# Kernel optimization log

Hardware: AMD Instinct MI355X
Metric: run time of the kernel (lower is better)

Reference implementation:

```python
import jax, jax.numpy as jnp
import numpy as np

CUTOFF = 5.2   # ANI-style radial cutoff (Angstrom); module takes this as a python float
BOX = 100.0    # box edge length for ~100k atoms at liquid-like density


def setup_inputs() -> dict:
    key = jax.random.key(0)
    k1, k2, k3, k4, k5 = jax.random.split(key, 5)
    N = 100_000      # atoms (molecules=1)
    P = 6_400_000    # candidate neighbor pairs (~64 per atom)
    coordinates = jax.random.uniform(k1, (1, N, 3), jnp.float32) * BOX
    species = jax.random.randint(k2, (1, N), 0, 8)
    species = jnp.where(jax.random.uniform(k3, (1, N)) < 0.02, -1, species)
    neighbor_idxs = jax.random.randint(k4, (2, P), 0, N)
    # small PBC shift vectors
    shift_values = jax.random.normal(k5, (P, 3), jnp.float32) * 0.1
    return {"species": species, "coordinates": coordinates,
            "neighbor_idxs": neighbor_idxs, "shift_values": shift_values}


def reference(species, coordinates, neighbor_idxs, shift_values):
    """Fused gather -> diff -> norm -> (dummy-mask & cutoff) screen.

    Faithful to Neighborlist._screen_with_cutoff, except dynamic stream
    compaction (nonzero/index_select) is replaced by fixed-size masking
    (jit-compatible): screened-out pairs get indices=-1, distances=0,
    diff_vectors=0.
    """
    coords = coordinates.reshape(-1, 3)              # [N, 3]
    dummy = species.reshape(-1) == -1                # [N]
    i0, i1 = neighbor_idxs[0], neighbor_idxs[1]      # [P], [P]
    valid = ~(dummy[i0] | dummy[i1])                 # non-dummy pairs

    diff = coords[i0] - coords[i1] + shift_values    # [P, 3]
    dist_sq = jnp.sum(diff * diff, axis=-1)          # [P]
    nonzero = dist_sq > 0
    dist = jnp.where(nonzero, jnp.sqrt(jnp.where(nonzero, dist_sq, 1.0)), 0.0)

    keep = valid & (dist <= CUTOFF)                  # [P] screening mask
    indices = jnp.where(keep, neighbor_idxs, -1)     # [2, P]
    distances = jnp.where(keep, dist, 0.0)           # [P]
    diff_vectors = jnp.where(keep[:, None], diff, 0.0)  # [P, 3]
    return indices, distances, diff_vectors
```

## Files before the change

kernel.cpp:

```cpp
#include <hip/hip_runtime.h>
#include <math.h>

#define CUTOFF_F 5.2f
#define BLOCK 256
#define PPT 8
#define BP (BLOCK * PPT)

typedef float f32x4 __attribute__((ext_vector_type(4)));
typedef int   i32x4 __attribute__((ext_vector_type(4)));

__global__ __launch_bounds__(BLOCK) void pack_atoms_kernel(
    const int*   __restrict__ species,
    const float* __restrict__ coords,
    f32x4*       __restrict__ atoms,
    int N)
{
    const int n = blockIdx.x * blockDim.x + threadIdx.x;
    if (n >= N) return;
    f32x4 a;
    a.x = coords[3l*n]; a.y = coords[3l*n+1]; a.z = coords[3l*n+2];
    a.w = (species[n] == -1) ? -1.0f : 0.0f;
    atoms[n] = a;
}

__global__ __launch_bounds__(BLOCK) void nbr_screen8_lds_kernel(
    const f32x4* __restrict__ atoms,
    const int*   __restrict__ nbr,
    const float* __restrict__ shift,
    float*       __restrict__ out,
    int P)
{
    __shared__ f32x4 lds[6 * BLOCK];
    const int  tid = threadIdx.x;
    const long PB  = (long)blockIdx.x * BP;

    if (PB + BP <= P) {
        const long baseA = PB + (long)tid * 4;
        const long baseB = baseA + (long)BLOCK * 4;

        const i32x4 i0A = __builtin_nontemporal_load(
            reinterpret_cast<const i32x4*>(nbr + baseA));
        const i32x4 i1A = __builtin_nontemporal_load(
            reinterpret_cast<const i32x4*>(nbr + (long)P + baseA));
        const i32x4 i0B = __builtin_nontemporal_load(
            reinterpret_cast<const i32x4*>(nbr + baseB));
        const i32x4 i1B = __builtin_nontemporal_load(
            reinterpret_cast<const i32x4*>(nbr + (long)P + baseB));

        const f32x4* src = reinterpret_cast<const f32x4*>(shift + PB * 3);
        f32x4 sreg[6];
        #pragma unroll
        for (int q = 0; q < 6; ++q)
            sreg[q] = __builtin_nontemporal_load(src + q * BLOCK + tid);

        const int ia[8] = {i0A.x, i0A.y, i0A.z, i0A.w, i0B.x, i0B.y, i0B.z, i0B.w};
        const int ib[8] = {i1A.x, i1A.y, i1A.z, i1A.w, i1B.x, i1B.y, i1B.z, i1B.w};
        f32x4 A[8], B[8];
        #pragma unroll
        for (int k = 0; k < 8; ++k) { A[k] = atoms[ia[k]]; B[k] = atoms[ib[k]]; }

        #pragma unroll
        for (int q = 0; q < 6; ++q)
            lds[q * BLOCK + tid] = sreg[q];
        __syncthreads();

        const f32x4 sA0 = lds[tid*3+0], sA1 = lds[tid*3+1], sA2 = lds[tid*3+2];
        const f32x4 sB0 = lds[3*BLOCK + tid*3+0], sB1 = lds[3*BLOCK + tid*3+1],
                    sB2 = lds[3*BLOCK + tid*3+2];
        const float shf[24] = {sA0.x, sA0.y, sA0.z, sA0.w,
                               sA1.x, sA1.y, sA1.z, sA1.w,
                               sA2.x, sA2.y, sA2.z, sA2.w,
                               sB0.x, sB0.y, sB0.z, sB0.w,
                               sB1.x, sB1.y, sB1.z, sB1.w,
                               sB2.x, sB2.y, sB2.z, sB2.w};

        float oi0[8], oi1[8], od[8], dv[24];
        #pragma unroll
        for (int k = 0; k < 8; ++k) {
            const bool valid = (A[k].w == 0.0f) & (B[k].w == 0.0f);
            const float dx = (A[k].x - B[k].x) + shf[3*k];
            const float dy = (A[k].y - B[k].y) + shf[3*k+1];
            const float dz = (A[k].z - B[k].z) + shf[3*k+2];
            const float d2 = __fadd_rn(__fadd_rn(__fmul_rn(dx, dx),
                                                 __fmul_rn(dy, dy)),
                                       __fmul_rn(dz, dz));
            const float dist = (d2 > 0.0f) ? sqrtf(d2) : 0.0f;
            const bool keep = valid && (dist <= CUTOFF_F);
            oi0[k] = keep ? (float)ia[k] : -1.0f;
            oi1[k] = keep ? (float)ib[k] : -1.0f;
            od[k]  = keep ? dist : 0.0f;
            dv[3*k]   = keep ? dx : 0.0f;
            dv[3*k+1] = keep ? dy : 0.0f;
            dv[3*k+2] = keep ? dz : 0.0f;
        }

        f32x4 w;
        w.x = dv[0];  w.y = dv[1];  w.z = dv[2];  w.w = dv[3];  lds[tid*3+0] = w;
        w.x = dv[4];  w.y = dv[5];  w.z = dv[6];  w.w = dv[7];  lds[tid*3+1] = w;
        w.x = dv[8];  w.y = dv[9];  w.z = dv[10]; w.w = dv[11]; lds[tid*3+2] = w;
        w.x = dv[12]; w.y = dv[13]; w.z = dv[14]; w.w = dv[15]; lds[3*BLOCK + tid*3+0] = w;
        w.x = dv[16]; w.y = dv[17]; w.z = dv[18]; w.w = dv[19]; lds[3*BLOCK + tid*3+1] = w;
        w.x = dv[20]; w.y = dv[21]; w.z = dv[22]; w.w = dv[23]; lds[3*BLOCK + tid*3+2] = w;

        f32x4 v;
        f32x4* o0 = reinterpret_cast<f32x4*>(out);
        f32x4* o1 = reinterpret_cast<f32x4*>(out + (long)P);
        f32x4* o2 = reinterpret_cast<f32x4*>(out + 2l*P);
        v.x = oi0[0]; v.y = oi0[1]; v.z = oi0[2]; v.w = oi0[3];
        __builtin_nontemporal_store(v, o0 + (baseA >> 2));
        v.x = oi0[4]; v.y = oi0[5]; v.z = oi0[6]; v.w = oi0[7];
        __builtin_nontemporal_store(v, o0 + (baseB >> 2));
        v.x = oi1[0]; v.y = oi1[1]; v.z = oi1[2]; v.w = oi1[3];
        __builtin_nontemporal_store(v, o1 + (baseA >> 2));
        v.x = oi1[4]; v.y = oi1[5]; v.z = oi1[6]; v.w = oi1[7];
        __builtin_nontemporal_store(v, o1 + (baseB >> 2));
        v.x = od[0];  v.y = od[1];  v.z = od[2];  v.w = od[3];
        __builtin_nontemporal_store(v, o2 + (baseA >> 2));
        v.x = od[4];  v.y = od[5];  v.z = od[6];  v.w = od[7];
        __builtin_nontemporal_store(v, o2 + (baseB >> 2));

        __syncthreads();

        f32x4* dst = reinterpret_cast<f32x4*>(out + 3l*P + PB*3);
        #pragma unroll
        for (int q = 0; q < 6; ++q)
            __builtin_nontemporal_store(lds[q * BLOCK + tid],
                                        dst + q * BLOCK + tid);
    } else {
        for (long p = PB + tid; p < P; p += BLOCK) {
            const int a = nbr[p], b = nbr[(long)P + p];
            const f32x4 ca = atoms[a], cb = atoms[b];
            const bool valid = (ca.w == 0.0f) & (cb.w == 0.0f);
            const float dx = (ca.x - cb.x) + shift[p*3];
            const float dy = (ca.y - cb.y) + shift[p*3+1];
            const float dz = (ca.z - cb.z) + shift[p*3+2];
            const float d2 = __fadd_rn(__fadd_rn(__fmul_rn(dx, dx),
                                                 __fmul_rn(dy, dy)),
                                       __fmul_rn(dz, dz));
            const float dist = (d2 > 0.0f) ? sqrtf(d2) : 0.0f;
            const bool keep = valid && (dist <= CUTOFF_F);
            out[p]         = keep ? (float)a : -1.0f;
            out[(long)P+p] = keep ? (float)b : -1.0f;
            out[2l*P+p]    = keep ? dist : 0.0f;
            out[3l*P+p*3]   = keep ? dx : 0.0f;
            out[3l*P+p*3+1] = keep ? dy : 0.0f;
            out[3l*P+p*3+2] = keep ? dz : 0.0f;
        }
    }
}

extern "C" void kernel_launch(void* const* d_in, const int* in_sizes, int n_in,
                              void* d_out, int out_size, void* d_ws, size_t ws_size,
                              hipStream_t stream) {
    const int*   species = (const int*)  d_in[0];
    const float* coords  = (const float*)d_in[1];
    const int*   nbr     = (const int*)  d_in[2];
    const float* shift   = (const float*)d_in[3];
    float* out = (float*)d_out;

    const int N = in_sizes[0];
    const int P = in_sizes[2] / 2;

    f32x4* atoms = (f32x4*)d_ws;
    hipLaunchKernelGGL(pack_atoms_kernel, dim3((N + BLOCK - 1) / BLOCK),
                       dim3(BLOCK), 0, stream, species, coords, atoms, N);
    const int grid = (P + BP - 1) / BP;
    hipLaunchKernelGGL(nbr_screen8_lds_kernel, dim3(grid), dim3(BLOCK), 0,
                       stream, atoms, nbr, shift, out, P);
}
```

Before: 93.27 us.

## Convert screen kernel to persistent grid-stride loop with index prefetch

The screening kernel becomes persistent: a fixed grid of up to 1024 blocks walks tiles with a grid-stride loop. Inside the loop it prefetches the neighbor indices for the block's next tile while the current tile's gathers and stores are in flight. The goal is to hide the dependent-load latency of index-then-atom gathers, and to cut block launch and tail effects. In exchange, fewer waves are resident per tile and register pressure rises from the prefetched indices, which may lower occupancy and latency hiding.

```diff
diff --git a/kernel.cpp b/kernel.cpp
--- a/kernel.cpp
+++ b/kernel.cpp
@@ -23,7 +23,7 @@
     atoms[n] = a;
 }
 
-__global__ __launch_bounds__(BLOCK) void nbr_screen8_lds_kernel(
+__global__ __launch_bounds__(BLOCK) void nbr_screen_pipe_kernel(
     const f32x4* __restrict__ atoms,
     const int*   __restrict__ nbr,
     const float* __restrict__ shift,
@@ -31,120 +31,145 @@
     int P)
 {
     __shared__ f32x4 lds[6 * BLOCK];
-    const int  tid = threadIdx.x;
-    const long PB  = (long)blockIdx.x * BP;
+    const int tid    = threadIdx.x;
+    const int nTiles = (P + BP - 1) / BP;
+    const int t0     = blockIdx.x;
+    if (t0 >= nTiles) return;
 
-    if (PB + BP <= P) {
-        const long baseA = PB + (long)tid * 4;
-        const long baseB = baseA + (long)BLOCK * 4;
+    i32x4 c0A, c1A, c0B, c1B;
+    {
+        const long PB = (long)t0 * BP;
+        if (PB + BP <= P) {
+            const long baseA = PB + (long)tid * 4;
+            const long baseB = baseA + (long)BLOCK * 4;
+            c0A = __builtin_nontemporal_load(reinterpret_cast<const i32x4*>(nbr + baseA));
+            c1A = __builtin_nontemporal_load(reinterpret_cast<const i32x4*>(nbr + (long)P + baseA));
+            c0B = __builtin_nontemporal_load(reinterpret_cast<const i32x4*>(nbr + baseB));
+            c1B = __builtin_nontemporal_load(reinterpret_cast<const i32x4*>(nbr + (long)P + baseB));
+        }
+    }
 
-        const i32x4 i0A = __builtin_nontemporal_load(
-            reinterpret_cast<const i32x4*>(nbr + baseA));
-        const i32x4 i1A = __builtin_nontemporal_load(
-            reinterpret_cast<const i32x4*>(nbr + (long)P + baseA));
-        const i32x4 i0B = __builtin_nontemporal_load(
-            reinterpret_cast<const i32x4*>(nbr + baseB));
-        const i32x4 i1B = __builtin_nontemporal_load(
-            reinterpret_cast<const i32x4*>(nbr + (long)P + baseB));
+    for (int t = t0; t < nTiles; t += gridDim.x) {
+        const long PB = (long)t * BP;
+        if (PB + BP <= P) {
+            const long baseA = PB + (long)tid * 4;
+            const long baseB = baseA + (long)BLOCK * 4;
 
-        const f32x4* src = reinterpret_cast<const f32x4*>(shift + PB * 3);
-        f32x4 sreg[6];
-        #pragma unroll
-        for (int q = 0; q < 6; ++q)
-            sreg[q] = __builtin_nontemporal_load(src + q * BLOCK + tid);
+            const int ia[8] = {c0A.x, c0A.y, c0A.z, c0A.w, c0B.x, c0B.y, c0B.z, c0B.w};
+            const int ib[8] = {c1A.x, c1A.y, c1A.z, c1A.w, c1B.x, c1B.y, c1B.z, c1B.w};
 
-        const int ia[8] = {i0A.x, i0A.y, i0A.z, i0A.w, i0B.x, i0B.y, i0B.z, i0B.w};
-        const int ib[8] = {i1A.x, i1A.y, i1A.z, i1A.w, i1B.x, i1B.y, i1B.z, i1B.w};
-        f32x4 A[8], B[8];
-        #pragma unroll
-        for (int k = 0; k < 8; ++k) { A[k] = atoms[ia[k]]; B[k] = atoms[ib[k]]; }
+            f32x4 A[8], B[8];
+            #pragma unroll
+            for (int k = 0; k < 8; ++k) { A[k] = atoms[ia[k]]; B[k] = atoms[ib[k]]; }
 
-        #pragma unroll
-        for (int q = 0; q < 6; ++q)
-            lds[q * BLOCK + tid] = sreg[q];
-        __syncthreads();
+            const f32x4* src = reinterpret_cast<const f32x4*>(shift + PB * 3);
+            f32x4 sreg[6];
+            #pragma unroll
+            for (int q = 0; q < 6; ++q)
+                sreg[q] = __builtin_nontemporal_load(src + q * BLOCK + tid);
 
-        const f32x4 sA0 = lds[tid*3+0], sA1 = lds[tid*3+1], sA2 = lds[tid*3+2];
-        const f32x4 sB0 = lds[3*BLOCK + tid*3+0], sB1 = lds[3*BLOCK + tid*3+1],
-                    sB2 = lds[3*BLOCK + tid*3+2];
-        const float shf[24] = {sA0.x, sA0.y, sA0.z, sA0.w,
-                               sA1.x, sA1.y, sA1.z, sA1.w,
-                               sA2.x, sA2.y, sA2.z, sA2.w,
-                               sB0.x, sB0.y, sB0.z, sB0.w,
-                               sB1.x, sB1.y, sB1.z, sB1.w,
-                               sB2.x, sB2.y, sB2.z, sB2.w};
+            const int  tn   = t + gridDim.x;
+            const long PBn  = (long)tn * BP;
+            i32x4 n0A, n1A, n0B, n1B;
+            const bool pre = (PBn + BP <= P);
+            if (pre) {
+                const long bA = PBn + (long)tid * 4;
+                const long bB = bA + (long)BLOCK * 4;
+                n0A = __builtin_nontemporal_load(reinterpret_cast<const i32x4*>(nbr + bA));
+                n1A = __builtin_nontemporal_load(reinterpret_cast<const i32x4*>(nbr + (long)P + bA));
+                n0B = __builtin_nontemporal_load(reinterpret_cast<const i32x4*>(nbr + bB));
+                n1B = __builtin_nontemporal_load(reinterpret_cast<const i32x4*>(nbr + (long)P + bB));
+            }
 
-        float oi0[8], oi1[8], od[8], dv[24];
-        #pragma unroll
-        for (int k = 0; k < 8; ++k) {
-            const bool valid = (A[k].w == 0.0f) & (B[k].w == 0.0f);
-            const float dx = (A[k].x - B[k].x) + shf[3*k];
-            const float dy = (A[k].y - B[k].y) + shf[3*k+1];
-            const float dz = (A[k].z - B[k].z) + shf[3*k+2];
-            const float d2 = __fadd_rn(__fadd_rn(__fmul_rn(dx, dx),
-                                                 __fmul_rn(dy, dy)),
-                                       __fmul_rn(dz, dz));
-            const float dist = (d2 > 0.0f) ? sqrtf(d2) : 0.0f;
-            const bool keep = valid && (dist <= CUTOFF_F);
-            oi0[k] = keep ? (float)ia[k] : -1.0f;
-            oi1[k] = keep ? (float)ib[k] : -1.0f;
-            od[k]  = keep ? dist : 0.0f;
-            dv[3*k]   = keep ? dx : 0.0f;
-            dv[3*k+1] = keep ? dy : 0.0f;
-            dv[3*k+2] = keep ? dz : 0.0f;
-        }
+            #pragma unroll
+            for (int q = 0; q < 6; ++q)
+                lds[q * BLOCK + tid] = sreg[q];
+            __syncthreads();
 
-        f32x4 w;
-        w.x = dv[0];  w.y = dv[1];  w.z = dv[2];  w.w = dv[3];  lds[tid*3+0] = w;
-        w.x = dv[4];  w.y = dv[5];  w.z = dv[6];  w.w = dv[7];  lds[tid*3+1] = w;
-        w.x = dv[8];  w.y = dv[9];  w.z = dv[10]; w.w = dv[11]; lds[tid*3+2] = w;
-        w.x = dv[12]; w.y = dv[13]; w.z = dv[14]; w.w = dv[15]; lds[3*BLOCK + tid*3+0] = w;
-        w.x = dv[16]; w.y = dv[17]; w.z = dv[18]; w.w = dv[19]; lds[3*BLOCK + tid*3+1] = w;
-        w.x = dv[20]; w.y = dv[21]; w.z = dv[22]; w.w = dv[23]; lds[3*BLOCK + tid*3+2] = w;
+            const f32x4 sA0 = lds[tid*3+0], sA1 = lds[tid*3+1], sA2 = lds[tid*3+2];
+            const f32x4 sB0 = lds[3*BLOCK + tid*3+0], sB1 = lds[3*BLOCK + tid*3+1],
+                        sB2 = lds[3*BLOCK + tid*3+2];
+            const float shf[24] = {sA0.x, sA0.y, sA0.z, sA0.w,
+                                   sA1.x, sA1.y, sA1.z, sA1.w,
+                                   sA2.x, sA2.y, sA2.z, sA2.w,
+                                   sB0.x, sB0.y, sB0.z, sB0.w,
+                                   sB1.x, sB1.y, sB1.z, sB1.w,
+                                   sB2.x, sB2.y, sB2.z, sB2.w};
 
-        f32x4 v;
-        f32x4* o0 = reinterpret_cast<f32x4*>(out);
-        f32x4* o1 = reinterpret_cast<f32x4*>(out + (long)P);
-        f32x4* o2 = reinterpret_cast<f32x4*>(out + 2l*P);
-        v.x = oi0[0]; v.y = oi0[1]; v.z = oi0[2]; v.w = oi0[3];
-        __builtin_nontemporal_store(v, o0 + (baseA >> 2));
-        v.x = oi0[4]; v.y = oi0[5]; v.z = oi0[6]; v.w = oi0[7];
-        __builtin_nontemporal_store(v, o0 + (baseB >> 2));
-        v.x = oi1[0]; v.y = oi1[1]; v.z = oi1[2]; v.w = oi1[3];
-        __builtin_nontemporal_store(v, o1 + (baseA >> 2));
-        v.x = oi1[4]; v.y = oi1[5]; v.z = oi1[6]; v.w = oi1[7];
-        __builtin_nontemporal_store(v, o1 + (baseB >> 2));
-        v.x = od[0];  v.y = od[1];  v.z = od[2];  v.w = od[3];
-        __builtin_nontemporal_store(v, o2 + (baseA >> 2));
-        v.x = od[4];  v.y = od[5];  v.z = od[6];  v.w = od[7];
-        __builtin_nontemporal_store(v, o2 + (baseB >> 2));
+            float oi0[8], oi1[8], od[8], dv[24];
+            #pragma unroll
+            for (int k = 0; k < 8; ++k) {
+                const bool valid = (A[k].w == 0.0f) & (B[k].w == 0.0f);
+                const float dx = (A[k].x - B[k].x) + shf[3*k];
+                const float dy = (A[k].y - B[k].y) + shf[3*k+1];
+                const float dz = (A[k].z - B[k].z) + shf[3*k+2];
+                const float d2 = __fadd_rn(__fadd_rn(__fmul_rn(dx, dx),
+                                                     __fmul_rn(dy, dy)),
+                                           __fmul_rn(dz, dz));
+                const float dist = (d2 > 0.0f) ? sqrtf(d2) : 0.0f;
+                const bool keep = valid && (dist <= CUTOFF_F);
+                oi0[k] = keep ? (float)ia[k] : -1.0f;
+                oi1[k] = keep ? (float)ib[k] : -1.0f;
+                od[k]  = keep ? dist : 0.0f;
+                dv[3*k]   = keep ? dx : 0.0f;
+                dv[3*k+1] = keep ? dy : 0.0f;
+                dv[3*k+2] = keep ? dz : 0.0f;
+            }
 
-        __syncthreads();
+            f32x4 w;
+            w.x = dv[0];  w.y = dv[1];  w.z = dv[2];  w.w = dv[3];  lds[tid*3+0] = w;
+            w.x = dv[4];  w.y = dv[5];  w.z = dv[6];  w.w = dv[7];  lds[tid*3+1] = w;
+            w.x = dv[8];  w.y = dv[9];  w.z = dv[10]; w.w = dv[11]; lds[tid*3+2] = w;
+            w.x = dv[12]; w.y = dv[13]; w.z = dv[14]; w.w = dv[15]; lds[3*BLOCK + tid*3+0] = w;
+            w.x = dv[16]; w.y = dv[17]; w.z = dv[18]; w.w = dv[19]; lds[3*BLOCK + tid*3+1] = w;
+            w.x = dv[20]; w.y = dv[21]; w.z = dv[22]; w.w = dv[23]; lds[3*BLOCK + tid*3+2] = w;
 
-        f32x4* dst = reinterpret_cast<f32x4*>(out + 3l*P + PB*3);
-        #pragma unroll
-        for (int q = 0; q < 6; ++q)
-            __builtin_nontemporal_store(lds[q * BLOCK + tid],
-                                        dst + q * BLOCK + tid);
-    } else {
-        for (long p = PB + tid; p < P; p += BLOCK) {
-            const int a = nbr[p], b = nbr[(long)P + p];
-            const f32x4 ca = atoms[a], cb = atoms[b];
-            const bool valid = (ca.w == 0.0f) & (cb.w == 0.0f);
-            const float dx = (ca.x - cb.x) + shift[p*3];
-            const float dy = (ca.y - cb.y) + shift[p*3+1];
-            const float dz = (ca.z - cb.z) + shift[p*3+2];
-            const float d2 = __fadd_rn(__fadd_rn(__fmul_rn(dx, dx),
-                                                 __fmul_rn(dy, dy)),
-                                       __fmul_rn(dz, dz));
-            const float dist = (d2 > 0.0f) ? sqrtf(d2) : 0.0f;
-            const bool keep = valid && (dist <= CUTOFF_F);
-            out[p]         = keep ? (float)a : -1.0f;
-            out[(long)P+p] = keep ? (float)b : -1.0f;
-            out[2l*P+p]    = keep ? dist : 0.0f;
-            out[3l*P+p*3]   = keep ? dx : 0.0f;
-            out[3l*P+p*3+1] = keep ? dy : 0.0f;
-            out[3l*P+p*3+2] = keep ? dz : 0.0f;
+            f32x4 v;
+            f32x4* o0 = reinterpret_cast<f32x4*>(out);
+            f32x4* o1 = reinterpret_cast<f32x4*>(out + (long)P);
+            f32x4* o2 = reinterpret_cast<f32x4*>(out + 2l*P);
+            v.x = oi0[0]; v.y = oi0[1]; v.z = oi0[2]; v.w = oi0[3];
+            __builtin_nontemporal_store(v, o0 + (baseA >> 2));
+            v.x = oi0[4]; v.y = oi0[5]; v.z = oi0[6]; v.w = oi0[7];
+            __builtin_nontemporal_store(v, o0 + (baseB >> 2));
+            v.x = oi1[0]; v.y = oi1[1]; v.z = oi1[2]; v.w = oi1[3];
+            __builtin_nontemporal_store(v, o1 + (baseA >> 2));
+            v.x = oi1[4]; v.y = oi1[5]; v.z = oi1[6]; v.w = oi1[7];
+            __builtin_nontemporal_store(v, o1 + (baseB >> 2));
+            v.x = od[0];  v.y = od[1];  v.z = od[2];  v.w = od[3];
+            __builtin_nontemporal_store(v, o2 + (baseA >> 2));
+            v.x = od[4];  v.y = od[5];  v.z = od[6];  v.w = od[7];
+            __builtin_nontemporal_store(v, o2 + (baseB >> 2));
+
+            __syncthreads();
+
+            f32x4* dst = reinterpret_cast<f32x4*>(out + 3l*P + PB*3);
+            #pragma unroll
+            for (int q = 0; q < 6; ++q)
+                __builtin_nontemporal_store(lds[q * BLOCK + tid],
+                                            dst + q * BLOCK + tid);
+
+            if (pre) { c0A = n0A; c1A = n1A; c0B = n0B; c1B = n1B; }
+        } else {
+            for (long p = PB + tid; p < P; p += BLOCK) {
+                const int a = nbr[p], b = nbr[(long)P + p];
+                const f32x4 ca = atoms[a], cb = atoms[b];
+                const bool valid = (ca.w == 0.0f) & (cb.w == 0.0f);
+                const float dx = (ca.x - cb.x) + shift[p*3];
+                const float dy = (ca.y - cb.y) + shift[p*3+1];
+                const float dz = (ca.z - cb.z) + shift[p*3+2];
+                const float d2 = __fadd_rn(__fadd_rn(__fmul_rn(dx, dx),
+                                                     __fmul_rn(dy, dy)),
+                                           __fmul_rn(dz, dz));
+                const float dist = (d2 > 0.0f) ? sqrtf(d2) : 0.0f;
+                const bool keep = valid && (dist <= CUTOFF_F);
+                out[p]         = keep ? (float)a : -1.0f;
+                out[(long)P+p] = keep ? (float)b : -1.0f;
+                out[2l*P+p]    = keep ? dist : 0.0f;
+                out[3l*P+p*3]   = keep ? dx : 0.0f;
+                out[3l*P+p*3+1] = keep ? dy : 0.0f;
+                out[3l*P+p*3+2] = keep ? dz : 0.0f;
+            }
         }
     }
 }
@@ -164,7 +189,10 @@
     f32x4* atoms = (f32x4*)d_ws;
     hipLaunchKernelGGL(pack_atoms_kernel, dim3((N + BLOCK - 1) / BLOCK),
                        dim3(BLOCK), 0, stream, species, coords, atoms, N);
-    const int grid = (P + BP - 1) / BP;
-    hipLaunchKernelGGL(nbr_screen8_lds_kernel, dim3(grid), dim3(BLOCK), 0,
+
+    const int nTiles = (P + BP - 1) / BP;
+    int grid = 1024;
+    if (grid > nTiles) grid = nTiles;
+    hipLaunchKernelGGL(nbr_screen_pipe_kernel, dim3(grid), dim3(BLOCK), 0,
                        stream, atoms, nbr, shift, out, P);
 }
```

Result: no change. 93.12 us (median of 2 runs) (-0.2%).
